# Optimization experiments

Hardware: AMD Instinct MI355X
Metric: run time of the kernel (lower is better)

The kernel has to match this reference:

```python
import jax, jax.numpy as jnp
import numpy as np

TAU = 2.0      # LIFNode tau
VTH = 1.0      # default v_threshold
ALPHA = 2.0    # surrogate.ATan default alpha

@jax.custom_vjp
def spike_fn(x):
    # Heaviside forward, ATan surrogate backward
    return (x >= 0.0).astype(x.dtype)

def _spike_fwd(x):
    return spike_fn(x), x

def _spike_bwd(x, g):
    return (g * (ALPHA / 2.0) / (1.0 + (jnp.pi / 2.0 * ALPHA * x) ** 2),)

spike_fn.defvjp(_spike_fwd, _spike_bwd)

def lif_step(v, cur):
    # spikingjelly LIFNode, decay_input=True, v_reset=0.0, hard reset, detach_reset=True
    v = v + (cur - v) / TAU
    s = spike_fn(v - VTH)
    v = v * (1.0 - jax.lax.stop_gradient(s))
    return v, s

def setup_inputs() -> dict:
    key = jax.random.key(0)
    ks = jax.random.split(key, 9)
    B, C, S, M = 2048, 3, 101, 40
    D_in, H, D_out = C * M, 200, 12
    x = jax.random.normal(ks[0], (B, C, S, M), dtype=jnp.float32)
    def lin(k, fan_in, fan_out):
        bound = 1.0 / np.sqrt(fan_in)
        kw, kb = jax.random.split(k)
        W = jax.random.uniform(kw, (fan_in, fan_out), jnp.float32, -bound, bound)
        b = jax.random.uniform(kb, (fan_out,), jnp.float32, -bound, bound)
        return W, b
    W1, b1 = lin(ks[1], D_in, H)
    W2, b2 = lin(ks[2], H, H)
    W3, b3 = lin(ks[3], H, H)
    Wr, br = lin(ks[4], H, D_out)
    return {"x": x, "W1": W1, "b1": b1, "W2": W2, "b2": b2,
            "W3": W3, "b3": b3, "Wr": Wr, "br": br}

def reference(x, W1, b1, W2, b2, W3, b3, Wr, br):
    B, C, S, M = x.shape
    # [B,C,S,M] -> [S,B,C*M]
    xs = jnp.transpose(x, (2, 0, 1, 3)).reshape(S, B, C * M)
    H = W1.shape[1]
    v0 = jnp.zeros((B, H), dtype=x.dtype)

    def step(carry, xt):
        v1, v2, v3 = carry
        v1, s1 = lif_step(v1, xt @ W1 + b1)
        v2, s2 = lif_step(v2, s1 @ W2 + b2)
        v3, s3 = lif_step(v3, s2 @ W3 + b3)
        return (v1, v2, v3), s3 @ Wr + br

    _, outs = jax.lax.scan(step, (v0, v0, v0), xs)  # outs: [S,B,D_out]
    return jax.nn.log_softmax(outs.mean(axis=0), axis=1)
```

## Files before the change

### kernel.cpp

```cpp
#include <hip/hip_runtime.h>
#include <hip/hip_bf16.h>

typedef unsigned long long u64;
typedef __attribute__((ext_vector_type(8))) short short8;
typedef __attribute__((ext_vector_type(4))) float f32x4;

#define S_STEPS 101
#define BATCH   2048
#define DIN     120
#define HID     200
#define DOUT    12

__device__ __forceinline__ ushort f2bf(float f) {
  union { float f; unsigned u; } c; c.f = f;
  unsigned r = (c.u + 0x7FFFu + ((c.u >> 16) & 1u)) >> 16;
  return (ushort)r;
}
__device__ __forceinline__ float bf2f(ushort s) {
  union { unsigned u; float f; } c; c.u = ((unsigned)s) << 16;
  return c.f;
}

__global__ __launch_bounds__(256) void k_l1(
    const float* __restrict__ x, const float* __restrict__ W1,
    const float* __restrict__ b1, u64* __restrict__ s1m)
{
  __shared__ ushort A_sh[2][16 * 128];
  const int tid  = threadIdx.x;
  const int lane = tid & 63;
  const int w    = tid >> 6;
  const int b0   = blockIdx.x * 16;
  const int rr   = lane & 15;
  const int hi   = lane >> 4;

  short8 bfrag[4][4];
  float  bias[4];
#pragma unroll
  for (int nt = 0; nt < 4; ++nt) {
    const int n0 = w * 64 + nt * 16 + rr;
    bias[nt] = (n0 < HID) ? b1[n0] : 0.0f;
#pragma unroll
    for (int ks = 0; ks < 4; ++ks) {
      short8 bf = 0;
#pragma unroll
      for (int j = 0; j < 8; ++j) {
        const int k = ks * 32 + hi * 8 + j;
        float wv = (k < DIN && n0 < HID) ? W1[k * HID + n0] : 0.0f;
        bf[j] = (short)f2bf(wv);
      }
      bfrag[nt][ks] = bf;
    }
  }

  if (tid < 32) {
    const int buf = tid >> 4, r = tid & 15;
    const int byt = r * 256 + (240 ^ ((r & 7) << 4));
    *(short8*)((char*)&A_sh[buf][0] + byt) = (short8)0;
  }

  const bool ldr = (tid < 240);
  const int  seg = ldr ? tid / 5 : 0;
  const int  grp = ldr ? tid % 5 : 0;
  const int  br_ = seg / 3, cc = seg % 3;
  const float* src = x + ((size_t)(b0 + br_) * 3 + cc) * (S_STEPS * 40) + grp * 8;
  const int wbyte = br_ * 256 + ((((cc * 40 + grp * 8) * 2)) ^ ((br_ & 7) << 4));

  float4 p0 = {0,0,0,0}, p1 = {0,0,0,0};
  if (ldr) { p0 = *(const float4*)(src); p1 = *(const float4*)(src + 4); }
  if (ldr) {
    short8 a;
    a[0]=(short)f2bf(p0.x); a[1]=(short)f2bf(p0.y); a[2]=(short)f2bf(p0.z); a[3]=(short)f2bf(p0.w);
    a[4]=(short)f2bf(p1.x); a[5]=(short)f2bf(p1.y); a[6]=(short)f2bf(p1.z); a[7]=(short)f2bf(p1.w);
    *(short8*)((char*)&A_sh[0][0] + wbyte) = a;
  }

  float vst[4][4] = {{0,0,0,0},{0,0,0,0},{0,0,0,0},{0,0,0,0}};
  const int g  = lane >> 2;
  const int r_ = lane & 3;
  __syncthreads();

#pragma unroll 1
  for (int t = 0; t < S_STEPS; ++t) {
    const int buf = t & 1;
    if (t + 1 < S_STEPS && ldr) {
      p0 = *(const float4*)(src + (t + 1) * 40);
      p1 = *(const float4*)(src + (t + 1) * 40 + 4);
    }
    short8 af[4];
#pragma unroll
    for (int ks = 0; ks < 4; ++ks) {
      const int byt = rr * 256 + ((ks * 64 + hi * 16) ^ ((rr & 7) << 4));
      af[ks] = *(const short8*)((const char*)&A_sh[buf][0] + byt);
    }
    u64 word = 0;
#pragma unroll
    for (int nt = 0; nt < 4; ++nt) {
      f32x4 acc = {0.f, 0.f, 0.f, 0.f};
#pragma unroll
      for (int ks = 0; ks < 4; ++ks)
        acc = __builtin_amdgcn_mfma_f32_16x16x32_bf16(af[ks], bfrag[nt][ks], acc, 0, 0, 0);
      u64 q0, q1, q2, q3;
      { float v = vst[nt][0]; v += 0.5f*((acc[0]+bias[nt]) - v); bool sp = v>=1.0f; vst[nt][0] = sp?0.f:v; q0 = __ballot(sp); }
      { float v = vst[nt][1]; v += 0.5f*((acc[1]+bias[nt]) - v); bool sp = v>=1.0f; vst[nt][1] = sp?0.f:v; q1 = __ballot(sp); }
      { float v = vst[nt][2]; v += 0.5f*((acc[2]+bias[nt]) - v); bool sp = v>=1.0f; vst[nt][2] = sp?0.f:v; q2 = __ballot(sp); }
      { float v = vst[nt][3]; v += 0.5f*((acc[3]+bias[nt]) - v); bool sp = v>=1.0f; vst[nt][3] = sp?0.f:v; q3 = __ballot(sp); }
      const u64 sel = (r_ == 0) ? q0 : ((r_ == 1) ? q1 : ((r_ == 2) ? q2 : q3));
      word |= ((sel >> (g * 16)) & 0xFFFFull) << (nt * 16);
    }
    if (lane < 16)
      s1m[((size_t)t * BATCH + b0 + lane) * 4 + w] = word;
    __syncthreads();
    if (t + 1 < S_STEPS && ldr) {
      short8 a;
      a[0]=(short)f2bf(p0.x); a[1]=(short)f2bf(p0.y); a[2]=(short)f2bf(p0.z); a[3]=(short)f2bf(p0.w);
      a[4]=(short)f2bf(p1.x); a[5]=(short)f2bf(p1.y); a[6]=(short)f2bf(p1.z); a[7]=(short)f2bf(p1.w);
      *(short8*)((char*)&A_sh[buf ^ 1][0] + wbyte) = a;
    }
    __syncthreads();
  }
}

template <bool CNT>
__global__ __launch_bounds__(256) void k_rec(
    const float* __restrict__ W, const float* __restrict__ bias,
    const u64* __restrict__ min_, u64* __restrict__ mout,
    float* __restrict__ cnt)
{
  extern __shared__ ushort Ws[];
  const int tid  = threadIdx.x;
  const int b0   = blockIdx.x * 4;
  const int lane = tid & 63;
  const bool act = tid < HID;

  for (int idx = tid; idx < HID * HID; idx += 256) Ws[idx] = f2bf(W[idx]);
  const float bv = act ? bias[tid] : 0.0f;
  float v[4]  = {0, 0, 0, 0};
  float c4[4] = {0, 0, 0, 0};

  u64 nxt[4][4];
#pragma unroll
  for (int i = 0; i < 4; ++i)
#pragma unroll
    for (int w = 0; w < 4; ++w) nxt[i][w] = min_[((size_t)0 * BATCH + b0 + i) * 4 + w];
  __syncthreads();

#pragma unroll 1
  for (int t = 0; t < S_STEPS; ++t) {
    u64 mm[4][4];
#pragma unroll
    for (int i = 0; i < 4; ++i)
#pragma unroll
      for (int w = 0; w < 4; ++w) mm[i][w] = nxt[i][w];
    if (t + 1 < S_STEPS) {
      const u64* np = min_ + ((size_t)(t + 1) * BATCH + b0) * 4;
#pragma unroll
      for (int i = 0; i < 4; ++i)
#pragma unroll
        for (int w = 0; w < 4; ++w) nxt[i][w] = np[i * 4 + w];
    }

    float acc[4] = {bv, bv, bv, bv};
#pragma unroll
    for (int w = 0; w < 4; ++w) {
      while ((mm[0][w] | mm[1][w] | mm[2][w] | mm[3][w]) != 0ull) {
#pragma unroll
        for (int i = 0; i < 4; ++i) {
          u64 m = mm[i][w];
          if (m) {
            int k = __builtin_ctzll(m);
            mm[i][w] = m & (m - 1);
            acc[i] += bf2f(Ws[(w * 64 + k) * HID + tid]);
          }
        }
      }
    }

#pragma unroll
    for (int i = 0; i < 4; ++i) {
      v[i] = v[i] + 0.5f * (acc[i] - v[i]);
      bool sp = act && (v[i] >= 1.0f);
      if (sp) v[i] = 0.0f;
      if (CNT) c4[i] += sp ? 1.0f : 0.0f;
      u64 bal = __ballot(sp);
      if (mout && lane == 0)
        mout[((size_t)t * BATCH + b0 + i) * 4 + (tid >> 6)] = bal;
    }
  }

  if (CNT && act) {
#pragma unroll
    for (int i = 0; i < 4; ++i)
      cnt[(size_t)(b0 + i) * HID + tid] = c4[i];
  }
}

__global__ __launch_bounds__(256) void k_readout(
    const float* __restrict__ cnt, const float* __restrict__ Wr,
    const float* __restrict__ br, float* __restrict__ out)
{
  __shared__ float cs[64 * HID];
  __shared__ float Wrs[HID * DOUT];
  __shared__ float brs[DOUT];
  __shared__ float os[64 * DOUT];
  const int tid = threadIdx.x;
  const int b0  = blockIdx.x * 64;

#pragma unroll
  for (int r = 0; r < 50; ++r)
    cs[r * 256 + tid] = cnt[(size_t)b0 * HID + r * 256 + tid];
  for (int idx = tid; idx < HID * DOUT; idx += 256) Wrs[idx] = Wr[idx];
  if (tid < DOUT) brs[tid] = br[tid];
  __syncthreads();

#pragma unroll
  for (int rep = 0; rep < 3; ++rep) {
    int idx = rep * 256 + tid;
    int bl = idx / DOUT, j = idx % DOUT;
    float a = 0.0f;
    for (int k = 0; k < HID; ++k)
      a += cs[bl * HID + k] * Wrs[k * DOUT + j];
    os[idx] = a * (1.0f / 101.0f) + brs[j];
  }
  __syncthreads();

  if (tid < 64) {
    float o[DOUT];
#pragma unroll
    for (int j = 0; j < DOUT; ++j) o[j] = os[tid * DOUT + j];
    float mx = o[0];
#pragma unroll
    for (int j = 1; j < DOUT; ++j) mx = fmaxf(mx, o[j]);
    float s = 0.0f;
#pragma unroll
    for (int j = 0; j < DOUT; ++j) s += expf(o[j] - mx);
    float ls = logf(s);
    float* op = out + (size_t)(b0 + tid) * DOUT;
#pragma unroll
    for (int j = 0; j < DOUT; ++j) op[j] = o[j] - mx - ls;
  }
}

extern "C" void kernel_launch(void* const* d_in, const int* in_sizes, int n_in,
                              void* d_out, int out_size, void* d_ws, size_t ws_size,
                              hipStream_t stream)
{
  const float* x  = (const float*)d_in[0];
  const float* W1 = (const float*)d_in[1];
  const float* b1 = (const float*)d_in[2];
  const float* W2 = (const float*)d_in[3];
  const float* b2 = (const float*)d_in[4];
  const float* W3 = (const float*)d_in[5];
  const float* b3 = (const float*)d_in[6];
  const float* Wr = (const float*)d_in[7];
  const float* br = (const float*)d_in[8];
  float* out = (float*)d_out;

  char* wsp = (char*)d_ws;
  const size_t mbytes = (size_t)S_STEPS * BATCH * 4 * sizeof(u64);
  u64* s1m   = (u64*)(wsp);
  u64* s2m   = (u64*)(wsp + mbytes);
  float* cnt = (float*)(wsp + 2 * mbytes);

  {
    void (*f2)(const float*, const float*, const u64*, u64*, float*) = k_rec<false>;
    void (*f3)(const float*, const float*, const u64*, u64*, float*) = k_rec<true>;
    hipFuncSetAttribute((const void*)f2, hipFuncAttributeMaxDynamicSharedMemorySize, 80000);
    hipFuncSetAttribute((const void*)f3, hipFuncAttributeMaxDynamicSharedMemorySize, 80000);
  }

  k_l1<<<BATCH / 16, 256, 0, stream>>>(x, W1, b1, s1m);
  k_rec<false><<<BATCH / 4, 256, 80000, stream>>>(W2, b2, s1m, s2m, nullptr);
  k_rec<true ><<<BATCH / 4, 256, 80000, stream>>>(W3, b3, s2m, nullptr, cnt);
  k_readout<<<32, 256, 0, stream>>>(cnt, Wr, br, out);
}
```

Before: 379.5 us.

## Load L1 MFMA fragments directly from global and double batch rows per recurrent block

Layer-1 no longer stages the input through double-buffered LDS with two barriers per step. Each lane now loads its own A-fragment floats straight from global memory, with a two-step register prefetch, and packs them to bf16 with a vector convert. The recurrent layers process 8 batch rows per block instead of 4, so each block's bf16 weight copy into LDS is amortised over twice the rows, and the whole spike-mask history is preloaded into LDS. This trades more registers and LDS per block (about 106KB) and half as many blocks for fewer barriers and fewer weight conversions.

```diff
diff --git a/kernel.cpp b/kernel.cpp
--- a/kernel.cpp
+++ b/kernel.cpp
@@ -2,6 +2,7 @@
 #include <hip/hip_bf16.h>
 
 typedef unsigned long long u64;
+typedef unsigned int uint;
 typedef __attribute__((ext_vector_type(8))) short short8;
 typedef __attribute__((ext_vector_type(4))) float f32x4;
 
@@ -20,12 +21,16 @@
   union { unsigned u; float f; } c; c.u = ((unsigned)s) << 16;
   return c.f;
 }
+__device__ __forceinline__ uint pkbf(float a, float b) {
+  __hip_bfloat162 h = __float22bfloat162_rn(make_float2(a, b));
+  uint u; __builtin_memcpy(&u, &h, 4);
+  return u;
+}
 
 __global__ __launch_bounds__(256) void k_l1(
     const float* __restrict__ x, const float* __restrict__ W1,
     const float* __restrict__ b1, u64* __restrict__ s1m)
 {
-  __shared__ ushort A_sh[2][16 * 128];
   const int tid  = threadIdx.x;
   const int lane = tid & 63;
   const int w    = tid >> 6;
@@ -34,11 +39,11 @@
   const int hi   = lane >> 4;
 
   short8 bfrag[4][4];
-  float  bias[4];
+  float  bv[4];
 #pragma unroll
   for (int nt = 0; nt < 4; ++nt) {
     const int n0 = w * 64 + nt * 16 + rr;
-    bias[nt] = (n0 < HID) ? b1[n0] : 0.0f;
+    bv[nt] = (n0 < HID) ? b1[n0] : 0.0f;
 #pragma unroll
     for (int ks = 0; ks < 4; ++ks) {
       short8 bf = 0;
@@ -52,72 +57,76 @@
     }
   }
 
-  if (tid < 32) {
-    const int buf = tid >> 4, r = tid & 15;
-    const int byt = r * 256 + (240 ^ ((r & 7) << 4));
-    *(short8*)((char*)&A_sh[buf][0] + byt) = (short8)0;
-  }
-
-  const bool ldr = (tid < 240);
-  const int  seg = ldr ? tid / 5 : 0;
-  const int  grp = ldr ? tid % 5 : 0;
-  const int  br_ = seg / 3, cc = seg % 3;
-  const float* src = x + ((size_t)(b0 + br_) * 3 + cc) * (S_STEPS * 40) + grp * 8;
-  const int wbyte = br_ * 256 + ((((cc * 40 + grp * 8) * 2)) ^ ((br_ & 7) << 4));
-
-  float4 p0 = {0,0,0,0}, p1 = {0,0,0,0};
-  if (ldr) { p0 = *(const float4*)(src); p1 = *(const float4*)(src + 4); }
-  if (ldr) {
-    short8 a;
-    a[0]=(short)f2bf(p0.x); a[1]=(short)f2bf(p0.y); a[2]=(short)f2bf(p0.z); a[3]=(short)f2bf(p0.w);
-    a[4]=(short)f2bf(p1.x); a[5]=(short)f2bf(p1.y); a[6]=(short)f2bf(p1.z); a[7]=(short)f2bf(p1.w);
-    *(short8*)((char*)&A_sh[0][0] + wbyte) = a;
+  const float* bp[4];
+#pragma unroll
+  for (int ks = 0; ks < 4; ++ks) {
+    int k0 = ks * 32 + hi * 8;
+    int c = (k0 < DIN) ? (k0 / 40) : 0;
+    int m = (k0 < DIN) ? (k0 % 40) : 0;
+    bp[ks] = x + ((size_t)(b0 + rr) * 3 + c) * (S_STEPS * 40) + m;
+  }
+  const bool pad = (hi == 3);
+
+  float4 P0[4][2] = {}; float4 P1[4][2] = {};
+#pragma unroll
+  for (int ks = 0; ks < 4; ++ks) {
+    if (!(ks == 3 && pad)) {
+      P0[ks][0] = *(const float4*)(bp[ks]);      P0[ks][1] = *(const float4*)(bp[ks] + 4);
+      P1[ks][0] = *(const float4*)(bp[ks] + 40); P1[ks][1] = *(const float4*)(bp[ks] + 44);
+    }
   }
 
   float vst[4][4] = {{0,0,0,0},{0,0,0,0},{0,0,0,0},{0,0,0,0}};
   const int g  = lane >> 2;
   const int r_ = lane & 3;
-  __syncthreads();
+
+#define L1_STEP(P, T, PFT)                                                      \
+  {                                                                             \
+    short8 af[4];                                                               \
+    _Pragma("unroll")                                                           \
+    for (int ks = 0; ks < 4; ++ks) {                                            \
+      union { short8 s; uint u[4]; } cv;                                        \
+      cv.u[0] = pkbf(P[ks][0].x, P[ks][0].y);                                   \
+      cv.u[1] = pkbf(P[ks][0].z, P[ks][0].w);                                   \
+      cv.u[2] = pkbf(P[ks][1].x, P[ks][1].y);                                   \
+      cv.u[3] = pkbf(P[ks][1].z, P[ks][1].w);                                   \
+      af[ks] = cv.s;                                                            \
+    }                                                                           \
+    if ((PFT) < S_STEPS) {                                                      \
+      _Pragma("unroll")                                                         \
+      for (int ks = 0; ks < 4; ++ks)                                            \
+        if (!(ks == 3 && pad)) {                                                \
+          P[ks][0] = *(const float4*)(bp[ks] + (PFT) * 40);                     \
+          P[ks][1] = *(const float4*)(bp[ks] + (PFT) * 40 + 4);                 \
+        }                                                                       \
+    }                                                                           \
+    u64 word = 0;                                                               \
+    _Pragma("unroll")                                                           \
+    for (int nt = 0; nt < 4; ++nt) {                                            \
+      f32x4 acc = {bv[nt], bv[nt], bv[nt], bv[nt]};                             \
+      _Pragma("unroll")                                                         \
+      for (int ks = 0; ks < 4; ++ks)                                            \
+        acc = __builtin_amdgcn_mfma_f32_16x16x32_bf16(af[ks], bfrag[nt][ks],    \
+                                                      acc, 0, 0, 0);            \
+      u64 q0, q1, q2, q3;                                                       \
+      { float v = vst[nt][0]; v = fmaf(0.5f, acc[0] - v, v); bool sp = v >= 1.0f; vst[nt][0] = sp ? 0.f : v; q0 = __ballot(sp); } \
+      { float v = vst[nt][1]; v = fmaf(0.5f, acc[1] - v, v); bool sp = v >= 1.0f; vst[nt][1] = sp ? 0.f : v; q1 = __ballot(sp); } \
+      { float v = vst[nt][2]; v = fmaf(0.5f, acc[2] - v, v); bool sp = v >= 1.0f; vst[nt][2] = sp ? 0.f : v; q2 = __ballot(sp); } \
+      { float v = vst[nt][3]; v = fmaf(0.5f, acc[3] - v, v); bool sp = v >= 1.0f; vst[nt][3] = sp ? 0.f : v; q3 = __ballot(sp); } \
+      const u64 sel = (r_ == 0) ? q0 : ((r_ == 1) ? q1 : ((r_ == 2) ? q2 : q3)); \
+      word |= ((sel >> (g * 16)) & 0xFFFFull) << (nt * 16);                     \
+    }                                                                           \
+    if (lane < 16)                                                              \
+      s1m[((size_t)(T) * BATCH + b0 + lane) * 4 + w] = word;                    \
+  }
 
 #pragma unroll 1
-  for (int t = 0; t < S_STEPS; ++t) {
-    const int buf = t & 1;
-    if (t + 1 < S_STEPS && ldr) {
-      p0 = *(const float4*)(src + (t + 1) * 40);
-      p1 = *(const float4*)(src + (t + 1) * 40 + 4);
-    }
-    short8 af[4];
-#pragma unroll
-    for (int ks = 0; ks < 4; ++ks) {
-      const int byt = rr * 256 + ((ks * 64 + hi * 16) ^ ((rr & 7) << 4));
-      af[ks] = *(const short8*)((const char*)&A_sh[buf][0] + byt);
-    }
-    u64 word = 0;
-#pragma unroll
-    for (int nt = 0; nt < 4; ++nt) {
-      f32x4 acc = {0.f, 0.f, 0.f, 0.f};
-#pragma unroll
-      for (int ks = 0; ks < 4; ++ks)
-        acc = __builtin_amdgcn_mfma_f32_16x16x32_bf16(af[ks], bfrag[nt][ks], acc, 0, 0, 0);
-      u64 q0, q1, q2, q3;
-      { float v = vst[nt][0]; v += 0.5f*((acc[0]+bias[nt]) - v); bool sp = v>=1.0f; vst[nt][0] = sp?0.f:v; q0 = __ballot(sp); }
-      { float v = vst[nt][1]; v += 0.5f*((acc[1]+bias[nt]) - v); bool sp = v>=1.0f; vst[nt][1] = sp?0.f:v; q1 = __ballot(sp); }
-      { float v = vst[nt][2]; v += 0.5f*((acc[2]+bias[nt]) - v); bool sp = v>=1.0f; vst[nt][2] = sp?0.f:v; q2 = __ballot(sp); }
-      { float v = vst[nt][3]; v += 0.5f*((acc[3]+bias[nt]) - v); bool sp = v>=1.0f; vst[nt][3] = sp?0.f:v; q3 = __ballot(sp); }
-      const u64 sel = (r_ == 0) ? q0 : ((r_ == 1) ? q1 : ((r_ == 2) ? q2 : q3));
-      word |= ((sel >> (g * 16)) & 0xFFFFull) << (nt * 16);
-    }
-    if (lane < 16)
-      s1m[((size_t)t * BATCH + b0 + lane) * 4 + w] = word;
-    __syncthreads();
-    if (t + 1 < S_STEPS && ldr) {
-      short8 a;
-      a[0]=(short)f2bf(p0.x); a[1]=(short)f2bf(p0.y); a[2]=(short)f2bf(p0.z); a[3]=(short)f2bf(p0.w);
-      a[4]=(short)f2bf(p1.x); a[5]=(short)f2bf(p1.y); a[6]=(short)f2bf(p1.z); a[7]=(short)f2bf(p1.w);
-      *(short8*)((char*)&A_sh[buf ^ 1][0] + wbyte) = a;
-    }
-    __syncthreads();
-  }
+  for (int t = 0; t < S_STEPS - 1; t += 2) {
+    L1_STEP(P0, t,     t + 2);
+    L1_STEP(P1, t + 1, t + 3);
+  }
+  L1_STEP(P0, S_STEPS - 1, S_STEPS);
+#undef L1_STEP
 }
 
 template <bool CNT>
@@ -126,45 +135,43 @@
     const u64* __restrict__ min_, u64* __restrict__ mout,
     float* __restrict__ cnt)
 {
-  extern __shared__ ushort Ws[];
+  extern __shared__ char smem[];
+  ushort* Ws = (ushort*)smem;
+  u64*    Ms = (u64*)(smem + 80000);
   const int tid  = threadIdx.x;
-  const int b0   = blockIdx.x * 4;
+  const int b0   = blockIdx.x * 8;
   const int lane = tid & 63;
   const bool act = tid < HID;
 
   for (int idx = tid; idx < HID * HID; idx += 256) Ws[idx] = f2bf(W[idx]);
+  {
+    const u64* gm = min_ + (size_t)b0 * 4;
+    for (int j = tid; j < S_STEPS * 32; j += 256) {
+      const int t = j >> 5, r = j & 31;
+      Ms[j] = gm[(size_t)t * (BATCH * 4) + r];
+    }
+  }
   const float bv = act ? bias[tid] : 0.0f;
-  float v[4]  = {0, 0, 0, 0};
-  float c4[4] = {0, 0, 0, 0};
-
-  u64 nxt[4][4];
-#pragma unroll
-  for (int i = 0; i < 4; ++i)
-#pragma unroll
-    for (int w = 0; w < 4; ++w) nxt[i][w] = min_[((size_t)0 * BATCH + b0 + i) * 4 + w];
+  float v[8]  = {0,0,0,0,0,0,0,0};
+  float c8[8] = {0,0,0,0,0,0,0,0};
   __syncthreads();
 
 #pragma unroll 1
   for (int t = 0; t < S_STEPS; ++t) {
-    u64 mm[4][4];
-#pragma unroll
-    for (int i = 0; i < 4; ++i)
-#pragma unroll
-      for (int w = 0; w < 4; ++w) mm[i][w] = nxt[i][w];
-    if (t + 1 < S_STEPS) {
-      const u64* np = min_ + ((size_t)(t + 1) * BATCH + b0) * 4;
-#pragma unroll
-      for (int i = 0; i < 4; ++i)
-#pragma unroll
-        for (int w = 0; w < 4; ++w) nxt[i][w] = np[i * 4 + w];
-    }
-
-    float acc[4] = {bv, bv, bv, bv};
+    const u64* mrow = Ms + t * 32;
+    u64 mm[8][4];
+#pragma unroll
+    for (int i = 0; i < 8; ++i)
+#pragma unroll
+      for (int w = 0; w < 4; ++w) mm[i][w] = mrow[i * 4 + w];
+
+    float acc[8] = {bv, bv, bv, bv, bv, bv, bv, bv};
 #pragma unroll
     for (int w = 0; w < 4; ++w) {
-      while ((mm[0][w] | mm[1][w] | mm[2][w] | mm[3][w]) != 0ull) {
-#pragma unroll
-        for (int i = 0; i < 4; ++i) {
+      while ((mm[0][w] | mm[1][w] | mm[2][w] | mm[3][w] |
+              mm[4][w] | mm[5][w] | mm[6][w] | mm[7][w]) != 0ull) {
+#pragma unroll
+        for (int i = 0; i < 8; ++i) {
           u64 m = mm[i][w];
           if (m) {
             int k = __builtin_ctzll(m);
@@ -176,11 +183,12 @@
     }
 
 #pragma unroll
-    for (int i = 0; i < 4; ++i) {
-      v[i] = v[i] + 0.5f * (acc[i] - v[i]);
-      bool sp = act && (v[i] >= 1.0f);
-      if (sp) v[i] = 0.0f;
-      if (CNT) c4[i] += sp ? 1.0f : 0.0f;
+    for (int i = 0; i < 8; ++i) {
+      float vv = v[i];
+      vv = fmaf(0.5f, acc[i] - vv, vv);
+      bool sp = act && (vv >= 1.0f);
+      v[i] = sp ? 0.0f : vv;
+      if (CNT) c8[i] += sp ? 1.0f : 0.0f;
       u64 bal = __ballot(sp);
       if (mout && lane == 0)
         mout[((size_t)t * BATCH + b0 + i) * 4 + (tid >> 6)] = bal;
@@ -189,8 +197,8 @@
 
   if (CNT && act) {
 #pragma unroll
-    for (int i = 0; i < 4; ++i)
-      cnt[(size_t)(b0 + i) * HID + tid] = c4[i];
+    for (int i = 0; i < 8; ++i)
+      cnt[(size_t)(b0 + i) * HID + tid] = c8[i];
   }
 }
 
@@ -261,15 +269,16 @@
   u64* s2m   = (u64*)(wsp + mbytes);
   float* cnt = (float*)(wsp + 2 * mbytes);
 
+  const int rec_lds = 80000 + S_STEPS * 32 * 8;
   {
     void (*f2)(const float*, const float*, const u64*, u64*, float*) = k_rec<false>;
     void (*f3)(const float*, const float*, const u64*, u64*, float*) = k_rec<true>;
-    hipFuncSetAttribute((const void*)f2, hipFuncAttributeMaxDynamicSharedMemorySize, 80000);
-    hipFuncSetAttribute((const void*)f3, hipFuncAttributeMaxDynamicSharedMemorySize, 80000);
+    hipFuncSetAttribute((const void*)f2, hipFuncAttributeMaxDynamicSharedMemorySize, rec_lds);
+    hipFuncSetAttribute((const void*)f3, hipFuncAttributeMaxDynamicSharedMemorySize, rec_lds);
   }
 
   k_l1<<<BATCH / 16, 256, 0, stream>>>(x, W1, b1, s1m);
-  k_rec<false><<<BATCH / 4, 256, 80000, stream>>>(W2, b2, s1m, s2m, nullptr);
-  k_rec<true ><<<BATCH / 4, 256, 80000, stream>>>(W3, b3, s2m, nullptr, cnt);
+  k_rec<false><<<BATCH / 8, 256, rec_lds, stream>>>(W2, b2, s1m, s2m, nullptr);
+  k_rec<true ><<<BATCH / 8, 256, rec_lds, stream>>>(W3, b3, s2m, nullptr, cnt);
   k_readout<<<32, 256, 0, stream>>>(cnt, Wr, br, out);
 }
```

New measurement: 543.0 us. +43.1%, slower.

## Fuse layer-2, layer-3 and readout into one kernel; widen layer-1 to 512 threads

Applied to the files above, without the earlier changes.

Layers 2 and 3 of the spiking scan and the readout plus log-softmax now run in a single kernel. Both recurrent weight matrices sit in LDS (about 160 KB), and layer-2 spike masks pass to layer 3 through shared memory instead of a global round trip. Layer 1 now uses 512 threads with 8 waves of 32 neurons each and a three-step register prefetch of x. Its spike masks are stored in a transposed uint layout so the fused kernel can load them with coalesced wide reads and scan bits with readfirstlane, and layer 3 is skipped in any step where layer 2 emitted no spikes. The fused kernel's large LDS footprint limits it to one block per CU with 256 blocks, so occupancy and latency hiding may suffer.

```diff
diff --git a/kernel.cpp b/kernel.cpp
--- a/kernel.cpp
+++ b/kernel.cpp
@@ -2,6 +2,7 @@
 #include <hip/hip_bf16.h>
 
 typedef unsigned long long u64;
+typedef unsigned int uint;
 typedef __attribute__((ext_vector_type(8))) short short8;
 typedef __attribute__((ext_vector_type(4))) float f32x4;
 
@@ -20,10 +21,15 @@
   union { unsigned u; float f; } c; c.u = ((unsigned)s) << 16;
   return c.f;
 }
-
-__global__ __launch_bounds__(256) void k_l1(
+__device__ __forceinline__ uint pkbf(float a, float b) {
+  __hip_bfloat162 h = __float22bfloat162_rn(make_float2(a, b));
+  uint u; __builtin_memcpy(&u, &h, 4);
+  return u;
+}
+
+__global__ __launch_bounds__(512) void k_l1(
     const float* __restrict__ x, const float* __restrict__ W1,
-    const float* __restrict__ b1, u64* __restrict__ s1m)
+    const float* __restrict__ b1, uint* __restrict__ m1)
 {
   __shared__ ushort A_sh[2][16 * 128];
   const int tid  = threadIdx.x;
@@ -33,12 +39,12 @@
   const int rr   = lane & 15;
   const int hi   = lane >> 4;
 
-  short8 bfrag[4][4];
-  float  bias[4];
-#pragma unroll
-  for (int nt = 0; nt < 4; ++nt) {
-    const int n0 = w * 64 + nt * 16 + rr;
-    bias[nt] = (n0 < HID) ? b1[n0] : 0.0f;
+  short8 bfrag[2][4];
+  float  bv[2];
+#pragma unroll
+  for (int p = 0; p < 2; ++p) {
+    const int n0 = w * 32 + p * 16 + rr;
+    bv[p] = (n0 < HID) ? b1[n0] : 0.0f;
 #pragma unroll
     for (int ks = 0; ks < 4; ++ks) {
       short8 bf = 0;
@@ -48,185 +54,212 @@
         float wv = (k < DIN && n0 < HID) ? W1[k * HID + n0] : 0.0f;
         bf[j] = (short)f2bf(wv);
       }
-      bfrag[nt][ks] = bf;
+      bfrag[p][ks] = bf;
     }
   }
 
   if (tid < 32) {
-    const int buf = tid >> 4, r = tid & 15;
-    const int byt = r * 256 + (240 ^ ((r & 7) << 4));
-    *(short8*)((char*)&A_sh[buf][0] + byt) = (short8)0;
-  }
-
-  const bool ldr = (tid < 240);
-  const int  seg = ldr ? tid / 5 : 0;
-  const int  grp = ldr ? tid % 5 : 0;
-  const int  br_ = seg / 3, cc = seg % 3;
-  const float* src = x + ((size_t)(b0 + br_) * 3 + cc) * (S_STEPS * 40) + grp * 8;
-  const int wbyte = br_ * 256 + ((((cc * 40 + grp * 8) * 2)) ^ ((br_ & 7) << 4));
-
-  float4 p0 = {0,0,0,0}, p1 = {0,0,0,0};
-  if (ldr) { p0 = *(const float4*)(src); p1 = *(const float4*)(src + 4); }
+    const int bu = tid >> 4, r = tid & 15;
+    *(short8*)((char*)&A_sh[bu][0] + r * 256 + (240 ^ ((r & 7) << 4))) = (short8)0;
+  }
+
+  const bool ldr = tid < 480;
+  int lb = 0, lc = 0, lg = 0;
+  if (ldr) { lb = tid / 30; int rem = tid % 30; lc = rem / 10; lg = rem % 10; }
+  const float* src = x + ((size_t)(b0 + lb) * 3 + lc) * (S_STEPS * 40) + lg * 4;
+  const int wbyte = lb * 256 + (((lc * 40 + lg * 4) * 2) ^ ((lb & 7) << 4));
+
+  float4 f1 = {0, 0, 0, 0}, f2 = {0, 0, 0, 0};
   if (ldr) {
-    short8 a;
-    a[0]=(short)f2bf(p0.x); a[1]=(short)f2bf(p0.y); a[2]=(short)f2bf(p0.z); a[3]=(short)f2bf(p0.w);
-    a[4]=(short)f2bf(p1.x); a[5]=(short)f2bf(p1.y); a[6]=(short)f2bf(p1.z); a[7]=(short)f2bf(p1.w);
-    *(short8*)((char*)&A_sh[0][0] + wbyte) = a;
-  }
-
-  float vst[4][4] = {{0,0,0,0},{0,0,0,0},{0,0,0,0},{0,0,0,0}};
-  const int g  = lane >> 2;
-  const int r_ = lane & 3;
+    float4 f0 = *(const float4*)src;
+    uint2 u; u.x = pkbf(f0.x, f0.y); u.y = pkbf(f0.z, f0.w);
+    *(uint2*)((char*)&A_sh[0][0] + wbyte) = u;
+    f1 = *(const float4*)(src + 40);
+    f2 = *(const float4*)(src + 80);
+  }
+
+  float vst[2][4] = {{0, 0, 0, 0}, {0, 0, 0, 0}};
+  const int pg = lane >> 2, pr = lane & 3;
   __syncthreads();
 
 #pragma unroll 1
   for (int t = 0; t < S_STEPS; ++t) {
-    const int buf = t & 1;
-    if (t + 1 < S_STEPS && ldr) {
-      p0 = *(const float4*)(src + (t + 1) * 40);
-      p1 = *(const float4*)(src + (t + 1) * 40 + 4);
-    }
+    const int cur = t & 1;
     short8 af[4];
 #pragma unroll
-    for (int ks = 0; ks < 4; ++ks) {
-      const int byt = rr * 256 + ((ks * 64 + hi * 16) ^ ((rr & 7) << 4));
-      af[ks] = *(const short8*)((const char*)&A_sh[buf][0] + byt);
-    }
-    u64 word = 0;
-#pragma unroll
-    for (int nt = 0; nt < 4; ++nt) {
-      f32x4 acc = {0.f, 0.f, 0.f, 0.f};
+    for (int ks = 0; ks < 4; ++ks)
+      af[ks] = *(const short8*)((const char*)&A_sh[cur][0] +
+                                rr * 256 + ((ks * 64 + hi * 16) ^ ((rr & 7) << 4)));
+    uint word = 0;
+#pragma unroll
+    for (int p = 0; p < 2; ++p) {
+      f32x4 acc = {bv[p], bv[p], bv[p], bv[p]};
 #pragma unroll
       for (int ks = 0; ks < 4; ++ks)
-        acc = __builtin_amdgcn_mfma_f32_16x16x32_bf16(af[ks], bfrag[nt][ks], acc, 0, 0, 0);
+        acc = __builtin_amdgcn_mfma_f32_16x16x32_bf16(af[ks], bfrag[p][ks], acc, 0, 0, 0);
       u64 q0, q1, q2, q3;
-      { float v = vst[nt][0]; v += 0.5f*((acc[0]+bias[nt]) - v); bool sp = v>=1.0f; vst[nt][0] = sp?0.f:v; q0 = __ballot(sp); }
-      { float v = vst[nt][1]; v += 0.5f*((acc[1]+bias[nt]) - v); bool sp = v>=1.0f; vst[nt][1] = sp?0.f:v; q1 = __ballot(sp); }
-      { float v = vst[nt][2]; v += 0.5f*((acc[2]+bias[nt]) - v); bool sp = v>=1.0f; vst[nt][2] = sp?0.f:v; q2 = __ballot(sp); }
-      { float v = vst[nt][3]; v += 0.5f*((acc[3]+bias[nt]) - v); bool sp = v>=1.0f; vst[nt][3] = sp?0.f:v; q3 = __ballot(sp); }
-      const u64 sel = (r_ == 0) ? q0 : ((r_ == 1) ? q1 : ((r_ == 2) ? q2 : q3));
-      word |= ((sel >> (g * 16)) & 0xFFFFull) << (nt * 16);
+      { float v = vst[p][0]; v = fmaf(0.5f, acc[0] - v, v); bool sp = v >= 1.0f; vst[p][0] = sp ? 0.f : v; q0 = __ballot(sp); }
+      { float v = vst[p][1]; v = fmaf(0.5f, acc[1] - v, v); bool sp = v >= 1.0f; vst[p][1] = sp ? 0.f : v; q1 = __ballot(sp); }
+      { float v = vst[p][2]; v = fmaf(0.5f, acc[2] - v, v); bool sp = v >= 1.0f; vst[p][2] = sp ? 0.f : v; q2 = __ballot(sp); }
+      { float v = vst[p][3]; v = fmaf(0.5f, acc[3] - v, v); bool sp = v >= 1.0f; vst[p][3] = sp ? 0.f : v; q3 = __ballot(sp); }
+      const u64 sel = (pr == 0) ? q0 : ((pr == 1) ? q1 : ((pr == 2) ? q2 : q3));
+      word |= (uint)((sel >> (pg * 16)) & 0xFFFFull) << (p * 16);
     }
     if (lane < 16)
-      s1m[((size_t)t * BATCH + b0 + lane) * 4 + w] = word;
+      m1[((size_t)t * 8 + w) * BATCH + b0 + lane] = word;
+
+    if (ldr) {
+      float4 wv4 = f1; f1 = f2;
+      if (t + 3 < S_STEPS) f2 = *(const float4*)(src + (t + 3) * 40);
+      if (t + 1 < S_STEPS) {
+        uint2 u; u.x = pkbf(wv4.x, wv4.y); u.y = pkbf(wv4.z, wv4.w);
+        *(uint2*)((char*)&A_sh[cur ^ 1][0] + wbyte) = u;
+      }
+    }
     __syncthreads();
-    if (t + 1 < S_STEPS && ldr) {
-      short8 a;
-      a[0]=(short)f2bf(p0.x); a[1]=(short)f2bf(p0.y); a[2]=(short)f2bf(p0.z); a[3]=(short)f2bf(p0.w);
-      a[4]=(short)f2bf(p1.x); a[5]=(short)f2bf(p1.y); a[6]=(short)f2bf(p1.z); a[7]=(short)f2bf(p1.w);
-      *(short8*)((char*)&A_sh[buf ^ 1][0] + wbyte) = a;
-    }
-    __syncthreads();
-  }
-}
-
-template <bool CNT>
-__global__ __launch_bounds__(256) void k_rec(
-    const float* __restrict__ W, const float* __restrict__ bias,
-    const u64* __restrict__ min_, u64* __restrict__ mout,
-    float* __restrict__ cnt)
+  }
+}
+
+__global__ __launch_bounds__(256) void k_scanrec(
+    const float* __restrict__ W2, const float* __restrict__ b2,
+    const float* __restrict__ W3, const float* __restrict__ b3,
+    const float* __restrict__ Wr, const float* __restrict__ br,
+    const uint* __restrict__ m1, float* __restrict__ out)
 {
-  extern __shared__ ushort Ws[];
+  extern __shared__ char smem[];
+  ushort* W2s = (ushort*)smem;
+  ushort* W3s = (ushort*)(smem + 80000);
+  u64*    ex  = (u64*)(smem + 160000);
+  float*  red = (float*)(smem + 160256);
+  int*    anyf = (int*)(smem + 160640);
+
   const int tid  = threadIdx.x;
-  const int b0   = blockIdx.x * 4;
   const int lane = tid & 63;
+  const int wv   = tid >> 6;
+  const int b0   = blockIdx.x * 8;
   const bool act = tid < HID;
 
-  for (int idx = tid; idx < HID * HID; idx += 256) Ws[idx] = f2bf(W[idx]);
-  const float bv = act ? bias[tid] : 0.0f;
-  float v[4]  = {0, 0, 0, 0};
-  float c4[4] = {0, 0, 0, 0};
-
-  u64 nxt[4][4];
-#pragma unroll
-  for (int i = 0; i < 4; ++i)
-#pragma unroll
-    for (int w = 0; w < 4; ++w) nxt[i][w] = min_[((size_t)0 * BATCH + b0 + i) * 4 + w];
+  {
+    const float4* g = (const float4*)W2;
+#pragma unroll 4
+    for (int i = tid; i < (HID * HID) / 4; i += 256) {
+      float4 v = g[i];
+      uint2 u; u.x = pkbf(v.x, v.y); u.y = pkbf(v.z, v.w);
+      *(uint2*)&W2s[i * 4] = u;
+    }
+  }
+  {
+    const float4* g = (const float4*)W3;
+#pragma unroll 4
+    for (int i = tid; i < (HID * HID) / 4; i += 256) {
+      float4 v = g[i];
+      uint2 u; u.x = pkbf(v.x, v.y); u.y = pkbf(v.z, v.w);
+      *(uint2*)&W3s[i * 4] = u;
+    }
+  }
+  if (tid == 0) { anyf[0] = 0; anyf[1] = 0; }
+
+  const float bias2 = act ? b2[tid] : 0.0f;
+  const float bias3 = act ? b3[tid] : 0.0f;
+  float v2[8] = {0,0,0,0,0,0,0,0};
+  float v3[8] = {0,0,0,0,0,0,0,0};
+  float cnt[8] = {0,0,0,0,0,0,0,0};
+
+  uint4 nxa[8], nxb[8];
+#pragma unroll
+  for (int ww = 0; ww < 8; ++ww) {
+    const uint* mp = m1 + (size_t)ww * BATCH + b0;
+    nxa[ww] = *(const uint4*)mp;
+    nxb[ww] = *(const uint4*)(mp + 4);
+  }
   __syncthreads();
 
 #pragma unroll 1
   for (int t = 0; t < S_STEPS; ++t) {
-    u64 mm[4][4];
-#pragma unroll
-    for (int i = 0; i < 4; ++i)
-#pragma unroll
-      for (int w = 0; w < 4; ++w) mm[i][w] = nxt[i][w];
+    uint4 ca[8], cb[8];
+#pragma unroll
+    for (int ww = 0; ww < 8; ++ww) { ca[ww] = nxa[ww]; cb[ww] = nxb[ww]; }
     if (t + 1 < S_STEPS) {
-      const u64* np = min_ + ((size_t)(t + 1) * BATCH + b0) * 4;
-#pragma unroll
-      for (int i = 0; i < 4; ++i)
-#pragma unroll
-        for (int w = 0; w < 4; ++w) nxt[i][w] = np[i * 4 + w];
-    }
-
-    float acc[4] = {bv, bv, bv, bv};
-#pragma unroll
-    for (int w = 0; w < 4; ++w) {
-      while ((mm[0][w] | mm[1][w] | mm[2][w] | mm[3][w]) != 0ull) {
-#pragma unroll
-        for (int i = 0; i < 4; ++i) {
-          u64 m = mm[i][w];
-          if (m) {
-            int k = __builtin_ctzll(m);
-            mm[i][w] = m & (m - 1);
-            acc[i] += bf2f(Ws[(w * 64 + k) * HID + tid]);
-          }
+#pragma unroll
+      for (int ww = 0; ww < 8; ++ww) {
+        const uint* mp = m1 + ((size_t)(t + 1) * 8 + ww) * BATCH + b0;
+        nxa[ww] = *(const uint4*)mp;
+        nxb[ww] = *(const uint4*)(mp + 4);
+      }
+    }
+
+    float a2[8];
+#pragma unroll
+    for (int i = 0; i < 8; ++i) a2[i] = bias2;
+#define SP2(VAL, I)                                                            \
+    { uint q = __builtin_amdgcn_readfirstlane(VAL);                            \
+      while (q) { int k = ww * 32 + __builtin_ctz(q); q &= q - 1;              \
+                  a2[I] += bf2f(W2s[k * HID + tid]); } }
+#pragma unroll
+    for (int ww = 0; ww < 8; ++ww) {
+      SP2(ca[ww].x, 0) SP2(ca[ww].y, 1) SP2(ca[ww].z, 2) SP2(ca[ww].w, 3)
+      SP2(cb[ww].x, 4) SP2(cb[ww].y, 5) SP2(cb[ww].z, 6) SP2(cb[ww].w, 7)
+    }
+#undef SP2
+
+#pragma unroll
+    for (int i = 0; i < 8; ++i) {
+      float vv = v2[i];
+      vv = fmaf(0.5f, a2[i] - vv, vv);
+      bool sp = act && (vv >= 1.0f);
+      v2[i] = sp ? 0.0f : vv;
+      u64 q = __ballot(sp);
+      if (lane == 0) { ex[i * 4 + wv] = q; if (q) anyf[t & 1] = 1; }
+    }
+    __syncthreads();
+    const int any2 = anyf[t & 1];
+    if (tid == 0) anyf[(t + 1) & 1] = 0;
+
+    float a3[8];
+#pragma unroll
+    for (int i = 0; i < 8; ++i) a3[i] = bias3;
+    if (any2) {
+#pragma unroll
+      for (int i = 0; i < 8; ++i) {
+#pragma unroll
+        for (int w4 = 0; w4 < 4; ++w4) {
+          u64 m = ex[i * 4 + w4];
+          uint qlo = __builtin_amdgcn_readfirstlane((uint)m);
+          uint qhi = __builtin_amdgcn_readfirstlane((uint)(m >> 32));
+          while (qlo) { int k = w4 * 64      + __builtin_ctz(qlo); qlo &= qlo - 1; a3[i] += bf2f(W3s[k * HID + tid]); }
+          while (qhi) { int k = w4 * 64 + 32 + __builtin_ctz(qhi); qhi &= qhi - 1; a3[i] += bf2f(W3s[k * HID + tid]); }
         }
       }
     }
-
-#pragma unroll
-    for (int i = 0; i < 4; ++i) {
-      v[i] = v[i] + 0.5f * (acc[i] - v[i]);
-      bool sp = act && (v[i] >= 1.0f);
-      if (sp) v[i] = 0.0f;
-      if (CNT) c4[i] += sp ? 1.0f : 0.0f;
-      u64 bal = __ballot(sp);
-      if (mout && lane == 0)
-        mout[((size_t)t * BATCH + b0 + i) * 4 + (tid >> 6)] = bal;
-    }
-  }
-
-  if (CNT && act) {
-#pragma unroll
-    for (int i = 0; i < 4; ++i)
-      cnt[(size_t)(b0 + i) * HID + tid] = c4[i];
-  }
-}
-
-__global__ __launch_bounds__(256) void k_readout(
-    const float* __restrict__ cnt, const float* __restrict__ Wr,
-    const float* __restrict__ br, float* __restrict__ out)
-{
-  __shared__ float cs[64 * HID];
-  __shared__ float Wrs[HID * DOUT];
-  __shared__ float brs[DOUT];
-  __shared__ float os[64 * DOUT];
-  const int tid = threadIdx.x;
-  const int b0  = blockIdx.x * 64;
-
-#pragma unroll
-  for (int r = 0; r < 50; ++r)
-    cs[r * 256 + tid] = cnt[(size_t)b0 * HID + r * 256 + tid];
-  for (int idx = tid; idx < HID * DOUT; idx += 256) Wrs[idx] = Wr[idx];
-  if (tid < DOUT) brs[tid] = br[tid];
-  __syncthreads();
-
-#pragma unroll
-  for (int rep = 0; rep < 3; ++rep) {
-    int idx = rep * 256 + tid;
-    int bl = idx / DOUT, j = idx % DOUT;
-    float a = 0.0f;
-    for (int k = 0; k < HID; ++k)
-      a += cs[bl * HID + k] * Wrs[k * DOUT + j];
-    os[idx] = a * (1.0f / 101.0f) + brs[j];
-  }
-  __syncthreads();
-
-  if (tid < 64) {
+#pragma unroll
+    for (int i = 0; i < 8; ++i) {
+      float vv = v3[i];
+      vv = fmaf(0.5f, a3[i] - vv, vv);
+      bool sp = act && (vv >= 1.0f);
+      v3[i] = sp ? 0.0f : vv;
+      cnt[i] += sp ? 1.0f : 0.0f;
+    }
+    __syncthreads();
+  }
+
+  if (tid < 96) red[tid] = 0.0f;
+  __syncthreads();
+  if (act) {
+    float wr[DOUT];
+#pragma unroll
+    for (int j = 0; j < DOUT; ++j) wr[j] = Wr[tid * DOUT + j];
+#pragma unroll
+    for (int i = 0; i < 8; ++i) {
+      float ci = cnt[i];
+#pragma unroll
+      for (int j = 0; j < DOUT; ++j) atomicAdd(&red[i * DOUT + j], ci * wr[j]);
+    }
+  }
+  __syncthreads();
+  if (tid < 8) {
     float o[DOUT];
 #pragma unroll
-    for (int j = 0; j < DOUT; ++j) o[j] = os[tid * DOUT + j];
+    for (int j = 0; j < DOUT; ++j) o[j] = red[tid * DOUT + j] * (1.0f / 101.0f) + br[j];
     float mx = o[0];
 #pragma unroll
     for (int j = 1; j < DOUT; ++j) mx = fmaxf(mx, o[j]);
@@ -255,21 +288,12 @@
   const float* br = (const float*)d_in[8];
   float* out = (float*)d_out;
 
-  char* wsp = (char*)d_ws;
-  const size_t mbytes = (size_t)S_STEPS * BATCH * 4 * sizeof(u64);
-  u64* s1m   = (u64*)(wsp);
-  u64* s2m   = (u64*)(wsp + mbytes);
-  float* cnt = (float*)(wsp + 2 * mbytes);
-
-  {
-    void (*f2)(const float*, const float*, const u64*, u64*, float*) = k_rec<false>;
-    void (*f3)(const float*, const float*, const u64*, u64*, float*) = k_rec<true>;
-    hipFuncSetAttribute((const void*)f2, hipFuncAttributeMaxDynamicSharedMemorySize, 80000);
-    hipFuncSetAttribute((const void*)f3, hipFuncAttributeMaxDynamicSharedMemorySize, 80000);
-  }
-
-  k_l1<<<BATCH / 16, 256, 0, stream>>>(x, W1, b1, s1m);
-  k_rec<false><<<BATCH / 4, 256, 80000, stream>>>(W2, b2, s1m, s2m, nullptr);
-  k_rec<true ><<<BATCH / 4, 256, 80000, stream>>>(W3, b3, s2m, nullptr, cnt);
-  k_readout<<<32, 256, 0, stream>>>(cnt, Wr, br, out);
-}
+  uint* m1 = (uint*)d_ws;
+
+  const int lds = 160648;
+  hipFuncSetAttribute((const void*)k_scanrec,
+                      hipFuncAttributeMaxDynamicSharedMemorySize, lds);
+
+  k_l1<<<BATCH / 16, 512, 0, stream>>>(x, W1, b1, m1);
+  k_scanrec<<<BATCH / 8, 256, lds, stream>>>(W2, b2, W3, b3, Wr, br, m1, out);
+}
```

Measured after the change: 764.4 us. +101.4%, slower.
